# Optimization experiments

Hardware: AMD Instinct MI355X
Metric: run time of the kernel (lower is better)

The kernel has to match this reference:

```python
import jax, jax.numpy as jnp
import numpy as np

B, I, O, C = 8192, 256, 256, 32


def setup_inputs() -> dict:
    key = jax.random.key(0)
    k1, k2, k3, k4 = jax.random.split(key, 4)
    x = jax.random.normal(k1, (B, I), dtype=jnp.float32)
    idx_channel = jax.random.randint(k2, (B,), 0, C, dtype=jnp.int64)
    # learned params per init_kwargs: weight [O, I, C], bias [O, C]
    weight = jax.random.normal(k3, (O, I, C), dtype=jnp.float32) * (1.0 / np.sqrt(I))
    bias = jax.random.normal(k4, (O, C), dtype=jnp.float32) * (1.0 / np.sqrt(O))
    return {"x": x, "idx_channel": idx_channel, "weight": weight, "bias": bias}


def reference(x, idx_channel, weight, bias):
    # Original: one_hot(idx) @ weight then batched matvec; mathematically this is
    # a per-sample gather of weight[..., idx[b]] followed by a batched GEMV + bias.
    w_sel = jnp.take(weight, idx_channel, axis=2)          # [O, I, B]
    b_sel = jnp.take(bias, idx_channel, axis=1).T          # [B, O]
    out = jnp.einsum('oib,bi->bo', w_sel, x) + b_sel       # [B, O]
    return out
```

## Files before the change

### kernel.cpp

```cpp
#include <hip/hip_runtime.h>
#include <hip/hip_bf16.h>

#define NB 8192
#define NI 256
#define NO 256
#define NC 32

typedef __attribute__((ext_vector_type(8))) short short8;
typedef __attribute__((ext_vector_type(4))) float floatx4;

#define WS_COUNTS_OFF 0
#define WS_LISTS_OFF  (4u << 10)
#define WS_WT_OFF     (1u << 20)

static __device__ __forceinline__ unsigned short f2bf(float f) {
    __hip_bfloat16 h = __float2bfloat16(f);
    return *(unsigned short*)&h;
}

#define PREP_TRAN 128
#define PREP_BLOCKS (PREP_TRAN + NC)

__global__ __launch_bounds__(256) void k_prep(
        const int* __restrict__ idx,
        const float* __restrict__ w,
        unsigned int* __restrict__ counts,
        unsigned short* __restrict__ lists,
        unsigned short* __restrict__ wT) {
    const int bid = blockIdx.x;
    const int tid = threadIdx.x;

    if (bid < PREP_TRAN) {
        int g0 = (bid * 256 + tid) * 2;
        const float4* s0 = (const float4*)(w + (size_t)g0 * NC);
        unsigned short v0[NC], v1[NC];
#pragma unroll
        for (int s = 0; s < 8; ++s) {
            float4 a = s0[s];
            v0[s * 4 + 0] = f2bf(a.x); v0[s * 4 + 1] = f2bf(a.y);
            v0[s * 4 + 2] = f2bf(a.z); v0[s * 4 + 3] = f2bf(a.w);
        }
#pragma unroll
        for (int s = 0; s < 8; ++s) {
            float4 a = s0[8 + s];
            v1[s * 4 + 0] = f2bf(a.x); v1[s * 4 + 1] = f2bf(a.y);
            v1[s * 4 + 2] = f2bf(a.z); v1[s * 4 + 3] = f2bf(a.w);
        }
#pragma unroll
        for (int c = 0; c < NC; ++c) {
            unsigned short pair[2] = {v0[c], v1[c]};
            *(unsigned int*)(wT + (size_t)c * (NO * NI) + g0) = *(unsigned int*)pair;
        }
    } else {
        __shared__ unsigned int lcnt;
        const int c = bid - PREP_TRAN;
        if (tid == 0) lcnt = 0u;
        __syncthreads();
        const int4* idx4 = (const int4*)idx;
        for (int t = tid; t < NB / 4; t += 256) {
            int4 v = idx4[t];
            int b0 = t * 4;
            if (v.x == c) lists[c * NB + atomicAdd(&lcnt, 1u)] = (unsigned short)(b0 + 0);
            if (v.y == c) lists[c * NB + atomicAdd(&lcnt, 1u)] = (unsigned short)(b0 + 1);
            if (v.z == c) lists[c * NB + atomicAdd(&lcnt, 1u)] = (unsigned short)(b0 + 2);
            if (v.w == c) lists[c * NB + atomicAdd(&lcnt, 1u)] = (unsigned short)(b0 + 3);
        }
        __syncthreads();
        if (tid == 0) counts[c] = lcnt;
    }
}

__launch_bounds__(256)
__global__ void k_gemm(const float* __restrict__ x,
                       const unsigned short* __restrict__ wT,
                       const float* __restrict__ bias,
                       const unsigned int* __restrict__ counts,
                       const unsigned short* __restrict__ lists,
                       float* __restrict__ out) {
    const int c  = blockIdx.x;
    const int o0 = blockIdx.y * 64;
    const int cnt = (int)counts[c];

    __shared__ unsigned short As[64][136];
    __shared__ unsigned short Bs[64][136];
    __shared__ int blist[64];

    const int tid  = threadIdx.x;
    const int wv   = tid >> 6;
    const int lane = tid & 63;
    const int lrc  = lane & 15;
    const int koff = (lane >> 4) * 8;
    const int rbase = (lane >> 4) * 4;

    const unsigned short* wTc = wT + ((size_t)c * NO + o0) * NI;
    const int o = o0 + wv * 16 + lrc;
    const float bv = bias[o * NC + c];

    for (int mt = blockIdx.z; mt * 64 < cnt; mt += 4) {
        const int m0 = mt * 64;
        if (tid < 64) {
            int mr = m0 + tid;
            blist[tid] = (int)lists[c * NB + (mr < cnt ? mr : m0)];
        }
        __syncthreads();

        floatx4 acc[4];
#pragma unroll
        for (int ms = 0; ms < 4; ++ms) acc[ms] = (floatx4){0.f, 0.f, 0.f, 0.f};

#pragma unroll
        for (int kt = 0; kt < 2; ++kt) {
            const int kb = kt * 128;
#pragma unroll
            for (int s = 0; s < 4; ++s) {
                int lin = tid + s * 256;
                int row = lin >> 4;
                int c8  = (lin & 15) * 8;
                const float4* pa = (const float4*)(x + (size_t)blist[row] * NI + kb + c8);
                float4 a0 = pa[0], a1 = pa[1];
                unsigned short r[8];
                r[0] = f2bf(a0.x); r[1] = f2bf(a0.y); r[2] = f2bf(a0.z); r[3] = f2bf(a0.w);
                r[4] = f2bf(a1.x); r[5] = f2bf(a1.y); r[6] = f2bf(a1.z); r[7] = f2bf(a1.w);
                *(uint4*)&As[row][c8] = *(uint4*)r;
                *(uint4*)&Bs[row][c8] = *(const uint4*)(wTc + (size_t)row * NI + kb + c8);
            }
            __syncthreads();

            const int n0 = wv * 16;
#pragma unroll
            for (int k0 = 0; k0 < 4; ++k0) {
                short8 bfrag = *(const short8*)&Bs[n0 + lrc][k0 * 32 + koff];
#pragma unroll
                for (int ms = 0; ms < 4; ++ms) {
                    short8 afrag = *(const short8*)&As[ms * 16 + lrc][k0 * 32 + koff];
                    acc[ms] = __builtin_amdgcn_mfma_f32_16x16x32_bf16(afrag, bfrag, acc[ms], 0, 0, 0);
                }
            }
            __syncthreads();
        }

#pragma unroll
        for (int ms = 0; ms < 4; ++ms) {
#pragma unroll
            for (int r = 0; r < 4; ++r) {
                int row = ms * 16 + rbase + r;
                if (m0 + row < cnt) {
                    out[(size_t)blist[row] * NO + o] = acc[ms][r] + bv;
                }
            }
        }
        __syncthreads();
    }
}

extern "C" void kernel_launch(void* const* d_in, const int* in_sizes, int n_in,
                              void* d_out, int out_size, void* d_ws, size_t ws_size,
                              hipStream_t stream) {
    const float* x    = (const float*)d_in[0];
    const int*   idx  = (const int*)d_in[1];
    const float* w    = (const float*)d_in[2];
    const float* bias = (const float*)d_in[3];
    float* out = (float*)d_out;

    char* ws = (char*)d_ws;
    unsigned int*   counts = (unsigned int*)(ws + WS_COUNTS_OFF);
    unsigned short* lists  = (unsigned short*)(ws + WS_LISTS_OFF);
    unsigned short* wT     = (unsigned short*)(ws + WS_WT_OFF);

    k_prep<<<PREP_BLOCKS, 256, 0, stream>>>(idx, w, counts, lists, wT);
    dim3 grid(NC, NO / 64, 4);
    k_gemm<<<grid, 256, 0, stream>>>(x, wT, bias, counts, lists, out);
}
```

Before: 83.03 us.

## Pre-convert x to bf16 and stage tiles via direct global-to-LDS loads with XOR swizzle

Adds a prep pass that converts x to bf16 into workspace, so the GEMM no longer converts each gathered row for every output-column block. The GEMM then loads whole 64x256 A and B tiles straight into LDS with global_load_lds, using an XOR-swizzled layout to avoid bank conflicts, and drops the two-stage K loop and its extra barriers. This trades an extra write and read of x in bf16 and larger LDS use per block (about 64KB) for fewer conversions and less register staging.

```diff
diff --git a/kernel.cpp b/kernel.cpp
--- a/kernel.cpp
+++ b/kernel.cpp
@@ -12,21 +12,32 @@
 #define WS_COUNTS_OFF 0
 #define WS_LISTS_OFF  (4u << 10)
 #define WS_WT_OFF     (1u << 20)
+#define WS_XBF_OFF    (5u << 20)
 
 static __device__ __forceinline__ unsigned short f2bf(float f) {
     __hip_bfloat16 h = __float2bfloat16(f);
     return *(unsigned short*)&h;
 }
 
+static __device__ __forceinline__ void gload_lds16(const void* g, void* l) {
+    __builtin_amdgcn_global_load_lds(
+        (const __attribute__((address_space(1))) unsigned int*)g,
+        (__attribute__((address_space(3))) unsigned int*)l,
+        16, 0, 0);
+}
+
 #define PREP_TRAN 128
-#define PREP_BLOCKS (PREP_TRAN + NC)
+#define PREP_XCONV 256
+#define PREP_BLOCKS (PREP_TRAN + NC + PREP_XCONV)
 
 __global__ __launch_bounds__(256) void k_prep(
         const int* __restrict__ idx,
         const float* __restrict__ w,
+        const float* __restrict__ x,
         unsigned int* __restrict__ counts,
         unsigned short* __restrict__ lists,
-        unsigned short* __restrict__ wT) {
+        unsigned short* __restrict__ wT,
+        unsigned short* __restrict__ xbf) {
     const int bid = blockIdx.x;
     const int tid = threadIdx.x;
 
@@ -51,7 +62,7 @@
             unsigned short pair[2] = {v0[c], v1[c]};
             *(unsigned int*)(wT + (size_t)c * (NO * NI) + g0) = *(unsigned int*)pair;
         }
-    } else {
+    } else if (bid < PREP_TRAN + NC) {
         __shared__ unsigned int lcnt;
         const int c = bid - PREP_TRAN;
         if (tid == 0) lcnt = 0u;
@@ -67,11 +78,24 @@
         }
         __syncthreads();
         if (tid == 0) counts[c] = lcnt;
+    } else {
+        int t = (bid - PREP_TRAN - NC) * 256 + tid;
+        const float4* src = (const float4*)(x + (size_t)t * 32);
+        __attribute__((aligned(16))) unsigned short v[32];
+#pragma unroll
+        for (int s = 0; s < 8; ++s) {
+            float4 a = src[s];
+            v[s * 4 + 0] = f2bf(a.x); v[s * 4 + 1] = f2bf(a.y);
+            v[s * 4 + 2] = f2bf(a.z); v[s * 4 + 3] = f2bf(a.w);
+        }
+        uint4* dst = (uint4*)(xbf + (size_t)t * 32);
+#pragma unroll
+        for (int s = 0; s < 4; ++s) dst[s] = ((const uint4*)v)[s];
     }
 }
 
 __launch_bounds__(256)
-__global__ void k_gemm(const float* __restrict__ x,
+__global__ void k_gemm(const unsigned short* __restrict__ xbf,
                        const unsigned short* __restrict__ wT,
                        const float* __restrict__ bias,
                        const unsigned int* __restrict__ counts,
@@ -81,20 +105,27 @@
     const int o0 = blockIdx.y * 64;
     const int cnt = (int)counts[c];
 
-    __shared__ unsigned short As[64][136];
-    __shared__ unsigned short Bs[64][136];
+    __shared__ unsigned short As[64 * 256];
+    __shared__ unsigned short Bs[64 * 256];
     __shared__ int blist[64];
 
     const int tid  = threadIdx.x;
     const int wv   = tid >> 6;
     const int lane = tid & 63;
     const int lrc  = lane & 15;
-    const int koff = (lane >> 4) * 8;
-    const int rbase = (lane >> 4) * 4;
+    const int hi   = lane >> 4;
+    const int hi16 = hi * 16;
+    const int X    = (lrc & 7) << 4;
+    const int rbase = hi * 4;
 
     const unsigned short* wTc = wT + ((size_t)c * NO + o0) * NI;
     const int o = o0 + wv * 16 + lrc;
     const float bv = bias[o * NC + c];
+
+    const int prow = tid >> 5;
+    const int e16  = (tid & 31) ^ prow;
+    const unsigned short* bsrc0 = wTc + prow * NI + e16 * 8;
+    const int dbase = wv * 512;
 
     for (int mt = blockIdx.z; mt * 64 < cnt; mt += 4) {
         const int m0 = mt * 64;
@@ -104,39 +135,32 @@
         }
         __syncthreads();
 
+#pragma unroll
+        for (int s = 0; s < 8; ++s)
+            gload_lds16(bsrc0 + s * 2048, Bs + dbase + s * 2048);
+#pragma unroll
+        for (int s = 0; s < 8; ++s) {
+            gload_lds16(xbf + (size_t)blist[s * 8 + prow] * NI + e16 * 8,
+                        As + dbase + s * 2048);
+        }
+        __syncthreads();
+
         floatx4 acc[4];
 #pragma unroll
         for (int ms = 0; ms < 4; ++ms) acc[ms] = (floatx4){0.f, 0.f, 0.f, 0.f};
 
+        const char* Ab = (const char*)As;
+        const char* Bb = (const char*)Bs;
+        const int nrow = wv * 16 + lrc;
 #pragma unroll
-        for (int kt = 0; kt < 2; ++kt) {
-            const int kb = kt * 128;
+        for (int k0 = 0; k0 < 8; ++k0) {
+            const int kx = ((k0 * 64) | hi16) ^ X;
+            short8 bfrag = *(const short8*)(Bb + nrow * 512 + kx);
 #pragma unroll
-            for (int s = 0; s < 4; ++s) {
-                int lin = tid + s * 256;
-                int row = lin >> 4;
-                int c8  = (lin & 15) * 8;
-                const float4* pa = (const float4*)(x + (size_t)blist[row] * NI + kb + c8);
-                float4 a0 = pa[0], a1 = pa[1];
-                unsigned short r[8];
-                r[0] = f2bf(a0.x); r[1] = f2bf(a0.y); r[2] = f2bf(a0.z); r[3] = f2bf(a0.w);
-                r[4] = f2bf(a1.x); r[5] = f2bf(a1.y); r[6] = f2bf(a1.z); r[7] = f2bf(a1.w);
-                *(uint4*)&As[row][c8] = *(uint4*)r;
-                *(uint4*)&Bs[row][c8] = *(const uint4*)(wTc + (size_t)row * NI + kb + c8);
+            for (int ms = 0; ms < 4; ++ms) {
+                short8 afrag = *(const short8*)(Ab + (ms * 16 + lrc) * 512 + kx);
+                acc[ms] = __builtin_amdgcn_mfma_f32_16x16x32_bf16(afrag, bfrag, acc[ms], 0, 0, 0);
             }
-            __syncthreads();
-
-            const int n0 = wv * 16;
-#pragma unroll
-            for (int k0 = 0; k0 < 4; ++k0) {
-                short8 bfrag = *(const short8*)&Bs[n0 + lrc][k0 * 32 + koff];
-#pragma unroll
-                for (int ms = 0; ms < 4; ++ms) {
-                    short8 afrag = *(const short8*)&As[ms * 16 + lrc][k0 * 32 + koff];
-                    acc[ms] = __builtin_amdgcn_mfma_f32_16x16x32_bf16(afrag, bfrag, acc[ms], 0, 0, 0);
-                }
-            }
-            __syncthreads();
         }
 
 #pragma unroll
@@ -166,8 +190,9 @@
     unsigned int*   counts = (unsigned int*)(ws + WS_COUNTS_OFF);
     unsigned short* lists  = (unsigned short*)(ws + WS_LISTS_OFF);
     unsigned short* wT     = (unsigned short*)(ws + WS_WT_OFF);
+    unsigned short* xbf    = (unsigned short*)(ws + WS_XBF_OFF);
 
-    k_prep<<<PREP_BLOCKS, 256, 0, stream>>>(idx, w, counts, lists, wT);
+    k_prep<<<PREP_BLOCKS, 256, 0, stream>>>(idx, w, x, counts, lists, wT, xbf);
     dim3 grid(NC, NO / 64, 4);
-    k_gemm<<<grid, 256, 0, stream>>>(x, wT, bias, counts, lists, out);
+    k_gemm<<<grid, 256, 0, stream>>>(xbf, wT, bias, counts, lists, out);
 }
```

Result: no change. 82.86 us (-0.2%).
